# Performance work log

Hardware: AMD Instinct MI355X
Metric: run time of the kernel (lower is better)

The kernel has to match this reference:

```python
import jax, jax.numpy as jnp
import numpy as np

CLASS_NUM = 2      # init_kwargs class_num
NUM_WEIGHTS = 3    # distinct values present in weighted_target (torch.unique)
SHAPE = (16, 2048, 2048)


def setup_inputs() -> dict:
    key = jax.random.key(0)
    k1, k2, k3 = jax.random.split(key, 3)
    pred = jax.random.uniform(k1, SHAPE, dtype=jnp.float32)
    target = jax.random.randint(k2, SHAPE, 0, CLASS_NUM).astype(jnp.int32)
    weighted_target = jax.random.randint(k3, SHAPE, 0, NUM_WEIGHTS).astype(jnp.int32)
    return {"pred": pred, "target": target, "weighted_target": weighted_target}


def reference(pred, target, weighted_target):
    # Original double loop over (class i, unique weight j):
    #   mask = (target==i) & (weighted_target==j); n = sum(mask)
    #   numerator   += sum(pred[mask]) / n^2
    #   denominator += sum((pred + mask)[mask]) / n^2 = (sum(pred[mask]) + n) / n^2
    # loss = 1 - 2*numerator/denominator
    # Single-pass segmented reduction over bucket id = class*W + weight.
    W = NUM_WEIGHTS
    nseg = CLASS_NUM * W
    seg = (target * W + weighted_target).reshape(-1)   # [N] bucket ids
    p = pred.reshape(-1)                               # [N]
    counts = jax.ops.segment_sum(jnp.ones_like(p), seg, num_segments=nseg)  # [nseg]
    psum = jax.ops.segment_sum(p, seg, num_segments=nseg)                   # [nseg]
    inv_n2 = jnp.where(counts > 0, 1.0 / (counts * counts), 0.0)
    numerator = jnp.sum(psum * inv_n2)
    denominator = jnp.sum((psum + counts) * inv_n2)
    return 1.0 - 2.0 * numerator / denominator
```

## Files before the change

### kernel.cpp

```cpp
#include <hip/hip_runtime.h>

#define NSEG 6
#define NBLOCKS 2048
#define NTHREADS 256

__device__ __forceinline__ void proc4(const float4& p, const int4& t, const int4& w,
                                      float ps[NSEG], unsigned long long& c64) {
    int s0 = t.x * 3 + w.x;
    int s1 = t.y * 3 + w.y;
    int s2 = t.z * 3 + w.z;
    int s3 = t.w * 3 + w.w;
    c64 += (1ull << (s0 << 3)) + (1ull << (s1 << 3)) +
           (1ull << (s2 << 3)) + (1ull << (s3 << 3));
#pragma unroll
    for (int s = 0; s < NSEG; ++s) {
        float v = (s0 == s ? p.x : 0.f);
        v += (s1 == s ? p.y : 0.f);
        v += (s2 == s ? p.z : 0.f);
        v += (s3 == s ? p.w : 0.f);
        ps[s] += v;
    }
}

__global__ __launch_bounds__(NTHREADS) void wdice_partial(
    const float4* __restrict__ pred,
    const int4* __restrict__ tgt,
    const int4* __restrict__ wt,
    int nvec,
    float* __restrict__ out_ws)
{
    float ps[NSEG];
    int cn[NSEG];
#pragma unroll
    for (int s = 0; s < NSEG; ++s) { ps[s] = 0.f; cn[s] = 0; }

    const int tid = threadIdx.x;
    const int stride = NBLOCKS * NTHREADS;
    int i = blockIdx.x * NTHREADS + tid;

    while (i + 3 * stride < nvec) {
        unsigned long long c64 = 0ull;
        for (int chunk = 0; chunk < 15 && i + 3 * stride < nvec; ++chunk, i += 4 * stride) {
            float4 p0 = pred[i];
            float4 p1 = pred[i + stride];
            float4 p2 = pred[i + 2 * stride];
            float4 p3 = pred[i + 3 * stride];
            int4 t0 = tgt[i];
            int4 t1 = tgt[i + stride];
            int4 t2 = tgt[i + 2 * stride];
            int4 t3 = tgt[i + 3 * stride];
            int4 w0 = wt[i];
            int4 w1 = wt[i + stride];
            int4 w2 = wt[i + 2 * stride];
            int4 w3 = wt[i + 3 * stride];

            proc4(p0, t0, w0, ps, c64);
            proc4(p1, t1, w1, ps, c64);
            proc4(p2, t2, w2, ps, c64);
            proc4(p3, t3, w3, ps, c64);
        }
#pragma unroll
        for (int s = 0; s < NSEG; ++s) cn[s] += (int)((c64 >> (8 * s)) & 0xFFull);
    }
    for (; i < nvec; i += stride) {
        float4 p = pred[i];
        int4 t = tgt[i];
        int4 w = wt[i];
        int s0 = t.x * 3 + w.x;
        int s1 = t.y * 3 + w.y;
        int s2 = t.z * 3 + w.z;
        int s3 = t.w * 3 + w.w;
#pragma unroll
        for (int s = 0; s < NSEG; ++s) {
            cn[s] += (s0 == s) + (s1 == s) + (s2 == s) + (s3 == s);
            float v = (s0 == s ? p.x : 0.f);
            v += (s1 == s ? p.y : 0.f);
            v += (s2 == s ? p.z : 0.f);
            v += (s3 == s ? p.w : 0.f);
            ps[s] += v;
        }
    }

    unsigned int pk0 = (unsigned)cn[0] | ((unsigned)cn[1] << 16);
    unsigned int pk1 = (unsigned)cn[2] | ((unsigned)cn[3] << 16);
    unsigned int pk2 = (unsigned)cn[4] | ((unsigned)cn[5] << 16);

#pragma unroll
    for (int off = 32; off > 0; off >>= 1) {
#pragma unroll
        for (int s = 0; s < NSEG; ++s) ps[s] += __shfl_down(ps[s], off, 64);
        pk0 += __shfl_down(pk0, off, 64);
        pk1 += __shfl_down(pk1, off, 64);
        pk2 += __shfl_down(pk2, off, 64);
    }

    __shared__ float lps[4][NSEG];
    __shared__ unsigned int lpk[4][3];
    int lane = tid & 63;
    int wave = tid >> 6;
    if (lane == 0) {
#pragma unroll
        for (int s = 0; s < NSEG; ++s) lps[wave][s] = ps[s];
        lpk[wave][0] = pk0; lpk[wave][1] = pk1; lpk[wave][2] = pk2;
    }
    __syncthreads();
    if (tid == 0) {
        unsigned int bk0 = lpk[0][0] + lpk[1][0] + lpk[2][0] + lpk[3][0];
        unsigned int bk1 = lpk[0][1] + lpk[1][1] + lpk[2][1] + lpk[3][1];
        unsigned int bk2 = lpk[0][2] + lpk[1][2] + lpk[2][2] + lpk[3][2];
#pragma unroll
        for (int s = 0; s < NSEG; ++s) {
            float tps = lps[0][s] + lps[1][s] + lps[2][s] + lps[3][s];
            out_ws[blockIdx.x * 12 + s] = tps;
        }
        out_ws[blockIdx.x * 12 + 6]  = (float)(bk0 & 0xFFFF);
        out_ws[blockIdx.x * 12 + 7]  = (float)(bk0 >> 16);
        out_ws[blockIdx.x * 12 + 8]  = (float)(bk1 & 0xFFFF);
        out_ws[blockIdx.x * 12 + 9]  = (float)(bk1 >> 16);
        out_ws[blockIdx.x * 12 + 10] = (float)(bk2 & 0xFFFF);
        out_ws[blockIdx.x * 12 + 11] = (float)(bk2 >> 16);
    }
}

__global__ __launch_bounds__(NTHREADS) void wdice_final(
    const float* __restrict__ ws,
    int nrows,
    float* __restrict__ out)
{
    double a[12];
#pragma unroll
    for (int r = 0; r < 12; ++r) a[r] = 0.0;

    for (int row = threadIdx.x; row < nrows; row += blockDim.x) {
#pragma unroll
        for (int r = 0; r < 12; ++r)
            a[r] += (double)ws[row * 12 + r];
    }

#pragma unroll
    for (int r = 0; r < 12; ++r) {
#pragma unroll
        for (int off = 32; off > 0; off >>= 1)
            a[r] += __shfl_down(a[r], off, 64);
    }

    __shared__ double l[4][12];
    int lane = threadIdx.x & 63;
    int wave = threadIdx.x >> 6;
    if (lane == 0) {
#pragma unroll
        for (int r = 0; r < 12; ++r) l[wave][r] = a[r];
    }
    __syncthreads();
    if (threadIdx.x == 0) {
        double numer = 0.0, denom = 0.0;
#pragma unroll
        for (int s = 0; s < NSEG; ++s) {
            double tps = l[0][s] + l[1][s] + l[2][s] + l[3][s];
            double tcn = l[0][s + 6] + l[1][s + 6] + l[2][s + 6] + l[3][s + 6];
            if (tcn > 0.0) {
                double inv_n2 = 1.0 / (tcn * tcn);
                numer += tps * inv_n2;
                denom += (tps + tcn) * inv_n2;
            }
        }
        out[0] = (float)(1.0 - 2.0 * numer / denom);
    }
}

extern "C" void kernel_launch(void* const* d_in, const int* in_sizes, int n_in,
                              void* d_out, int out_size, void* d_ws, size_t ws_size,
                              hipStream_t stream) {
    const float4* pred = (const float4*)d_in[0];
    const int4* tgt = (const int4*)d_in[1];
    const int4* wt = (const int4*)d_in[2];
    int n = in_sizes[0];
    int nvec = n / 4;

    float* ws = (float*)d_ws;

    wdice_partial<<<NBLOCKS, NTHREADS, 0, stream>>>(pred, tgt, wt, nvec, ws);
    wdice_final<<<1, NTHREADS, 0, stream>>>(ws, NBLOCKS, (float*)d_out);
}
```

Baseline: 152.5 us.

## Replace 4-way unrolled loads with double-buffered software pipeline in partial reduction

Replaces the loop that issues 12 vector loads per iteration with a two-stage software pipeline: the next float4/int4 triple is fetched while the current one is accumulated. Packed byte counters are flushed every 62 chunks rather than every 15 outer iterations. Launch bounds now ask for 8 blocks per SM to raise occupancy with lower register pressure. The cost is fewer loads in flight per thread, which may hurt memory-level parallelism on this bandwidth-bound reduction.

Result: slower. 228.7 us (+50.0%).

```diff
diff --git a/kernel.cpp b/kernel.cpp
--- a/kernel.cpp
+++ b/kernel.cpp
@@ -4,8 +4,8 @@
 #define NBLOCKS 2048
 #define NTHREADS 256
 
-__device__ __forceinline__ void proc4(const float4& p, const int4& t, const int4& w,
-                                      float ps[NSEG], unsigned long long& c64) {
+__device__ __forceinline__ void consume4(const float4 p, const int4 t, const int4 w,
+                                         float (&ps)[NSEG], unsigned long long& c64) {
     int s0 = t.x * 3 + w.x;
     int s1 = t.y * 3 + w.y;
     int s2 = t.z * 3 + w.z;
@@ -22,7 +22,16 @@
     }
 }
 
-__global__ __launch_bounds__(NTHREADS) void wdice_partial(
+#define FLUSH_C64()                                                   \
+    do {                                                              \
+        _Pragma("unroll")                                             \
+        for (int s = 0; s < NSEG; ++s)                                \
+            cn[s] += (int)((c64 >> (8 * s)) & 0xFFull);               \
+        c64 = 0ull;                                                   \
+        fl = 0;                                                       \
+    } while (0)
+
+__global__ __launch_bounds__(NTHREADS, 8) void wdice_partial(
     const float4* __restrict__ pred,
     const int4* __restrict__ tgt,
     const int4* __restrict__ wt,
@@ -33,53 +42,39 @@
     int cn[NSEG];
 #pragma unroll
     for (int s = 0; s < NSEG; ++s) { ps[s] = 0.f; cn[s] = 0; }
+    unsigned long long c64 = 0ull;
+    int fl = 0;
 
     const int tid = threadIdx.x;
     const int stride = NBLOCKS * NTHREADS;
     int i = blockIdx.x * NTHREADS + tid;
 
-    while (i + 3 * stride < nvec) {
-        unsigned long long c64 = 0ull;
-        for (int chunk = 0; chunk < 15 && i + 3 * stride < nvec; ++chunk, i += 4 * stride) {
-            float4 p0 = pred[i];
-            float4 p1 = pred[i + stride];
-            float4 p2 = pred[i + 2 * stride];
-            float4 p3 = pred[i + 3 * stride];
-            int4 t0 = tgt[i];
-            int4 t1 = tgt[i + stride];
-            int4 t2 = tgt[i + 2 * stride];
-            int4 t3 = tgt[i + 3 * stride];
-            int4 w0 = wt[i];
-            int4 w1 = wt[i + stride];
-            int4 w2 = wt[i + 2 * stride];
-            int4 w3 = wt[i + 3 * stride];
+    float4 pA, pB;
+    int4 tA, tB, wA, wB;
 
-            proc4(p0, t0, w0, ps, c64);
-            proc4(p1, t1, w1, ps, c64);
-            proc4(p2, t2, w2, ps, c64);
-            proc4(p3, t3, w3, ps, c64);
+    bool validA = (i < nvec);
+    if (validA) { pA = pred[i]; tA = tgt[i]; wA = wt[i]; }
+    int j = i + stride;
+
+    while (true) {
+        bool validB = (j < nvec);
+        if (validB) { pB = pred[j]; tB = tgt[j]; wB = wt[j]; }
+        if (validA) {
+            consume4(pA, tA, wA, ps, c64);
+            if (++fl == 62) FLUSH_C64();
         }
-#pragma unroll
-        for (int s = 0; s < NSEG; ++s) cn[s] += (int)((c64 >> (8 * s)) & 0xFFull);
+        if (!validB) break;
+
+        i = j + stride;
+        validA = (i < nvec);
+        if (validA) { pA = pred[i]; tA = tgt[i]; wA = wt[i]; }
+        consume4(pB, tB, wB, ps, c64);
+        if (++fl == 62) FLUSH_C64();
+        if (!validA) break;
+
+        j = i + stride;
     }
-    for (; i < nvec; i += stride) {
-        float4 p = pred[i];
-        int4 t = tgt[i];
-        int4 w = wt[i];
-        int s0 = t.x * 3 + w.x;
-        int s1 = t.y * 3 + w.y;
-        int s2 = t.z * 3 + w.z;
-        int s3 = t.w * 3 + w.w;
-#pragma unroll
-        for (int s = 0; s < NSEG; ++s) {
-            cn[s] += (s0 == s) + (s1 == s) + (s2 == s) + (s3 == s);
-            float v = (s0 == s ? p.x : 0.f);
-            v += (s1 == s ? p.y : 0.f);
-            v += (s2 == s ? p.z : 0.f);
-            v += (s3 == s ? p.w : 0.f);
-            ps[s] += v;
-        }
-    }
+    FLUSH_C64();
 
     unsigned int pk0 = (unsigned)cn[0] | ((unsigned)cn[1] << 16);
     unsigned int pk1 = (unsigned)cn[2] | ((unsigned)cn[3] << 16);
```

## Double-buffer input streams through LDS with async global_load_lds and fewer blocks

Applied to the files above, without the earlier changes.

Replaces the direct 4-way unrolled register loads with a per-wave double-buffered pipeline. Each iteration issues `global_load_lds` for the next tile of pred, target and weight straight into LDS, then waits with `s_waitcnt vmcnt(3)` and consumes the current tile from LDS. The grid drops from 2048 to 1536 blocks, and the packed-count flush interval is adjusted to 60 iterations. The goal is to overlap loads with compute, but each thread now has only three 16-byte loads in flight instead of twelve, which may cut memory-level parallelism for this bandwidth-bound reduction.

Result: no change. 153.0 us (+0.3%).

```diff
diff --git a/kernel.cpp b/kernel.cpp
--- a/kernel.cpp
+++ b/kernel.cpp
@@ -1,11 +1,16 @@
 #include <hip/hip_runtime.h>
 
 #define NSEG 6
-#define NBLOCKS 2048
+#define NBLOCKS 1536
 #define NTHREADS 256
 
-__device__ __forceinline__ void proc4(const float4& p, const int4& t, const int4& w,
-                                      float ps[NSEG], unsigned long long& c64) {
+typedef __attribute__((address_space(3))) void* lds_vp;
+typedef const __attribute__((address_space(1))) void* gl_vp;
+
+#define GLOAD16(g, l) __builtin_amdgcn_global_load_lds((gl_vp)(g), (lds_vp)(l), 16, 0, 0)
+
+__device__ __forceinline__ void consume4(const float4 p, const int4 t, const int4 w,
+                                         float (&ps)[NSEG], unsigned long long& c64) {
     int s0 = t.x * 3 + w.x;
     int s1 = t.y * 3 + w.y;
     int s2 = t.z * 3 + w.z;
@@ -29,57 +34,69 @@
     int nvec,
     float* __restrict__ out_ws)
 {
+    __shared__ float4 bp[2][NTHREADS];
+    __shared__ int4   bt[2][NTHREADS];
+    __shared__ int4   bw[2][NTHREADS];
+
+    const int tid = threadIdx.x;
+    const int lane = tid & 63;
+    const int wv = tid >> 6;
+    const int G = NBLOCKS * NTHREADS;
+
     float ps[NSEG];
     int cn[NSEG];
 #pragma unroll
     for (int s = 0; s < NSEG; ++s) { ps[s] = 0.f; cn[s] = 0; }
+    unsigned long long c64 = 0ull;
+    int fl = 0;
 
-    const int tid = threadIdx.x;
-    const int stride = NBLOCKS * NTHREADS;
-    int i = blockIdx.x * NTHREADS + tid;
+    const int vbase = blockIdx.x * NTHREADS + wv * 64;
+    int idx = vbase + lane;
+    int k = 0;
+    bool valid = (vbase + 64) <= nvec;
 
-    while (i + 3 * stride < nvec) {
-        unsigned long long c64 = 0ull;
-        for (int chunk = 0; chunk < 15 && i + 3 * stride < nvec; ++chunk, i += 4 * stride) {
-            float4 p0 = pred[i];
-            float4 p1 = pred[i + stride];
-            float4 p2 = pred[i + 2 * stride];
-            float4 p3 = pred[i + 3 * stride];
-            int4 t0 = tgt[i];
-            int4 t1 = tgt[i + stride];
-            int4 t2 = tgt[i + 2 * stride];
-            int4 t3 = tgt[i + 3 * stride];
-            int4 w0 = wt[i];
-            int4 w1 = wt[i + stride];
-            int4 w2 = wt[i + 2 * stride];
-            int4 w3 = wt[i + 3 * stride];
+    if (valid) {
+        GLOAD16(pred + idx, &bp[0][wv * 64]);
+        GLOAD16(tgt + idx,  &bt[0][wv * 64]);
+        GLOAD16(wt + idx,   &bw[0][wv * 64]);
+    }
 
-            proc4(p0, t0, w0, ps, c64);
-            proc4(p1, t1, w1, ps, c64);
-            proc4(p2, t2, w2, ps, c64);
-            proc4(p3, t3, w3, ps, c64);
+    while (valid) {
+        const int b = k & 1;
+        const int nidx = idx + G;
+        const bool validn = (vbase + (k + 1) * G + 64) <= nvec;
+        if (validn) {
+            GLOAD16(pred + nidx, &bp[b ^ 1][wv * 64]);
+            GLOAD16(tgt + nidx,  &bt[b ^ 1][wv * 64]);
+            GLOAD16(wt + nidx,   &bw[b ^ 1][wv * 64]);
+            asm volatile("s_waitcnt vmcnt(3)" ::: "memory");
+        } else {
+            asm volatile("s_waitcnt vmcnt(0)" ::: "memory");
         }
+        float4 p = bp[b][tid];
+        int4 t = bt[b][tid];
+        int4 w = bw[b][tid];
+        consume4(p, t, w, ps, c64);
+        if (++fl == 60) {
 #pragma unroll
-        for (int s = 0; s < NSEG; ++s) cn[s] += (int)((c64 >> (8 * s)) & 0xFFull);
+            for (int s = 0; s < NSEG; ++s) cn[s] += (int)((c64 >> (8 * s)) & 0xFFull);
+            c64 = 0ull; fl = 0;
+        }
+        idx = nidx; valid = validn; ++k;
     }
-    for (; i < nvec; i += stride) {
+#pragma unroll
+    for (int s = 0; s < NSEG; ++s) cn[s] += (int)((c64 >> (8 * s)) & 0xFFull);
+    c64 = 0ull;
+
+    const int tail = nvec & ~63;
+    for (int i = tail + blockIdx.x * NTHREADS + tid; i < nvec; i += G) {
         float4 p = pred[i];
         int4 t = tgt[i];
         int4 w = wt[i];
-        int s0 = t.x * 3 + w.x;
-        int s1 = t.y * 3 + w.y;
-        int s2 = t.z * 3 + w.z;
-        int s3 = t.w * 3 + w.w;
+        consume4(p, t, w, ps, c64);
+    }
 #pragma unroll
-        for (int s = 0; s < NSEG; ++s) {
-            cn[s] += (s0 == s) + (s1 == s) + (s2 == s) + (s3 == s);
-            float v = (s0 == s ? p.x : 0.f);
-            v += (s1 == s ? p.y : 0.f);
-            v += (s2 == s ? p.z : 0.f);
-            v += (s3 == s ? p.w : 0.f);
-            ps[s] += v;
-        }
-    }
+    for (int s = 0; s < NSEG; ++s) cn[s] += (int)((c64 >> (8 * s)) & 0xFFull);
 
     unsigned int pk0 = (unsigned)cn[0] | ((unsigned)cn[1] << 16);
     unsigned int pk1 = (unsigned)cn[2] | ((unsigned)cn[3] << 16);
@@ -96,12 +113,10 @@
 
     __shared__ float lps[4][NSEG];
     __shared__ unsigned int lpk[4][3];
-    int lane = tid & 63;
-    int wave = tid >> 6;
     if (lane == 0) {
 #pragma unroll
-        for (int s = 0; s < NSEG; ++s) lps[wave][s] = ps[s];
-        lpk[wave][0] = pk0; lpk[wave][1] = pk1; lpk[wave][2] = pk2;
+        for (int s = 0; s < NSEG; ++s) lps[wv][s] = ps[s];
+        lpk[wv][0] = pk0; lpk[wv][1] = pk1; lpk[wv][2] = pk2;
     }
     __syncthreads();
     if (tid == 0) {
```
